# Kernel optimization log

Measured on AMD Instinct MI355X. Metric: run time of the kernel, lower is better.

The kernel has to match this reference:

```python
import jax, jax.numpy as jnp
import numpy as np

EPS = 1e-5

def _ste(x, q):
    # straight-through estimator: forward = q, backward = identity
    return x + jax.lax.stop_gradient(q - x)

def quant_act_int4(x):
    # per-token absmax quantization to int4 range [-8, 7] (dequantized)
    s = jnp.clip(jnp.max(jnp.abs(x), axis=-1, keepdims=True), EPS, None) / 7.0
    q = jnp.clip(jnp.round(x / s), -8.0, 7.0) * s
    return _ste(x, q)

def ternary_weight(w):
    # absmean ternary quantization: scale = mean(|w|), w_q in {-1,0,+1} * scale
    scale = jnp.clip(jnp.mean(jnp.abs(w)), EPS, None)
    t = jnp.clip(jnp.round(w / scale), -1.0, 1.0)
    return _ste(w, t * scale)

def setup_inputs() -> dict:
    key = jax.random.key(0)
    kx, kw = jax.random.split(key)
    in_features, out_features = 4096, 16384
    x = jax.random.normal(kx, (4, 2048, in_features), dtype=jnp.float32)
    # kaiming_uniform_(a=sqrt(5)) -> U(-b, b), b = sqrt(6/((1+5)*fan_in)) = 1/sqrt(fan_in)
    bound = 1.0 / np.sqrt(in_features)
    latent_weight = jax.random.uniform(kw, (out_features, in_features), dtype=jnp.float32,
                                       minval=-bound, maxval=bound)
    return {"x": x, "latent_weight": latent_weight}

def reference(x, latent_weight):
    xq = quant_act_int4(x)                    # (B, S, in)
    w_eff = ternary_weight(latent_weight)     # (out, in)
    return jnp.einsum('bsi,oi->bso', xq, w_eff)
```

## Files before the change

### kernel.cpp

```cpp
#include <hip/hip_runtime.h>
#include <hip/hip_bf16.h>
#include <stdint.h>


#define K_DIM 4096
#define M_DIM 8192
#define N_DIM 16384

typedef int v4i __attribute__((ext_vector_type(4)));

typedef __attribute__((address_space(1))) void gvoid_t;
typedef __attribute__((address_space(3))) void lvoid_t;

__device__ __forceinline__ void gl_lds16(const void* g, void* l) {
    __builtin_amdgcn_global_load_lds((gvoid_t*)(void*)g, (lvoid_t*)l, 16, 0, 0);
}

__global__ __launch_bounds__(256) void wabs_partial_k(const float* __restrict__ w,
                                                      double* __restrict__ part) {
    const long n4 = (long)N_DIM * K_DIM / 4;
    long i = (long)blockIdx.x * blockDim.x + threadIdx.x;
    const long stride = (long)gridDim.x * blockDim.x;
    const float4* w4 = (const float4*)w;
    double s = 0.0;
    for (; i < n4; i += stride) {
        float4 v = w4[i];
        s += (double)fabsf(v.x);
        s += (double)fabsf(v.y);
        s += (double)fabsf(v.z);
        s += (double)fabsf(v.w);
    }
    __shared__ double red[256];
    const int tid = threadIdx.x;
    red[tid] = s;
    __syncthreads();
    for (int w2 = 128; w2 > 0; w2 >>= 1) {
        if (tid < w2) red[tid] += red[tid + w2];
        __syncthreads();
    }
    if (tid == 0) part[blockIdx.x] = red[0];
}

__global__ __launch_bounds__(256) void wscale_final_k(const double* __restrict__ part,
                                                      float* __restrict__ wscale) {
    __shared__ double red[256];
    const int tid = threadIdx.x;
    double s = 0.0;
    for (int i = tid; i < 1024; i += 256) s += part[i];
    red[tid] = s;
    __syncthreads();
    for (int w2 = 128; w2 > 0; w2 >>= 1) {
        if (tid < w2) red[tid] += red[tid + w2];
        __syncthreads();
    }
    if (tid == 0) {
        double mean = red[0] / (double)((long)N_DIM * K_DIM);
        *wscale = fmaxf((float)mean, 1e-5f);
    }
}

__global__ __launch_bounds__(256) void wquant_k(const float* __restrict__ w,
                                                signed char* __restrict__ qw,
                                                const float* __restrict__ wscale) {
    const float sc = *wscale;
    const long i = (long)blockIdx.x * 256 + threadIdx.x;
    const float4* w4 = (const float4*)(w + i * 16);
    union { signed char c[16]; int4 v; } u;
#pragma unroll
    for (int j = 0; j < 4; ++j) {
        float4 v = w4[j];
        u.c[j * 4 + 0] = (signed char)fminf(fmaxf(rintf(v.x / sc), -1.f), 1.f);
        u.c[j * 4 + 1] = (signed char)fminf(fmaxf(rintf(v.y / sc), -1.f), 1.f);
        u.c[j * 4 + 2] = (signed char)fminf(fmaxf(rintf(v.z / sc), -1.f), 1.f);
        u.c[j * 4 + 3] = (signed char)fminf(fmaxf(rintf(v.w / sc), -1.f), 1.f);
    }
    *(int4*)(qw + i * 16) = u.v;
}

__global__ __launch_bounds__(256) void xquant_k(const float* __restrict__ x,
                                                signed char* __restrict__ qx,
                                                float* __restrict__ sx,
                                                const float* __restrict__ wscale) {
    const int row = blockIdx.x;
    const int tid = threadIdx.x;
    const float4* xr = (const float4*)(x + (long)row * K_DIM) + tid * 4;
    float4 v[4];
    float am = 0.f;
#pragma unroll
    for (int j = 0; j < 4; ++j) {
        v[j] = xr[j];
        am = fmaxf(am, fmaxf(fmaxf(fabsf(v[j].x), fabsf(v[j].y)),
                             fmaxf(fabsf(v[j].z), fabsf(v[j].w))));
    }
#pragma unroll
    for (int off = 32; off > 0; off >>= 1) am = fmaxf(am, __shfl_down(am, off));
    __shared__ float wm[4];
    if ((tid & 63) == 0) wm[tid >> 6] = am;
    __syncthreads();
    am = fmaxf(fmaxf(wm[0], wm[1]), fmaxf(wm[2], wm[3]));
    const float s = fmaxf(am, 1e-5f) / 7.0f;
    union { signed char c[16]; int4 q; } u;
#pragma unroll
    for (int j = 0; j < 4; ++j) {
        u.c[j * 4 + 0] = (signed char)fminf(fmaxf(rintf(v[j].x / s), -8.f), 7.f);
        u.c[j * 4 + 1] = (signed char)fminf(fmaxf(rintf(v[j].y / s), -8.f), 7.f);
        u.c[j * 4 + 2] = (signed char)fminf(fmaxf(rintf(v[j].z / s), -8.f), 7.f);
        u.c[j * 4 + 3] = (signed char)fminf(fmaxf(rintf(v[j].w / s), -8.f), 7.f);
    }
    *(int4*)(qx + (long)row * K_DIM + tid * 16) = u.q;
    if (tid == 0) sx[row] = s * (*wscale);
}

__global__ __launch_bounds__(256) void gemm_k(const signed char* __restrict__ qx,
                                              const signed char* __restrict__ qw,
                                              const float* __restrict__ sx,
                                              float* __restrict__ out) {
    __shared__ signed char lA[128 * 64];
    __shared__ signed char lB[128 * 64];

    const int tid  = threadIdx.x;
    const int lane = tid & 63;
    const int wave = tid >> 6;
    const int m0 = blockIdx.x * 128;
    const int n0 = blockIdx.y * 128;
    const int wr = (wave >> 1) * 64;
    const int wc = (wave & 1) * 64;

    const int c0 = tid, c1 = tid + 256;
    const int r0 = c0 >> 2, r1 = c1 >> 2;
    const int g0 = ((c0 & 3) - ((r0 >> 1) & 3)) & 3;
    const int g1 = ((c1 & 3) - ((r1 >> 1) & 3)) & 3;
    const signed char* gA0 = qx + (long)(m0 + r0) * K_DIM + g0 * 16;
    const signed char* gA1 = qx + (long)(m0 + r1) * K_DIM + g1 * 16;
    const signed char* gB0 = qw + (long)(n0 + r0) * K_DIM + g0 * 16;
    const signed char* gB1 = qw + (long)(n0 + r1) * K_DIM + g1 * 16;
    signed char* lA0 = &lA[c0 * 16];
    signed char* lA1 = &lA[c1 * 16];
    signed char* lB0 = &lB[c0 * 16];
    signed char* lB1 = &lB[c1 * 16];

    const int fr = lane & 15;
    const int fq = lane >> 4;
    int offA[4], offB[4];
#pragma unroll
    for (int i = 0; i < 4; ++i) {
        int ra = wr + i * 16 + fr;
        offA[i] = ra * 64 + (((fq + (ra >> 1)) & 3) << 4);
        int rb = wc + i * 16 + fr;
        offB[i] = rb * 64 + (((fq + (rb >> 1)) & 3) << 4);
    }

    v4i acc[4][4];
#pragma unroll
    for (int i = 0; i < 4; ++i)
#pragma unroll
        for (int j = 0; j < 4; ++j) acc[i][j] = 0;

    for (int k0 = 0; k0 < K_DIM; k0 += 64) {
        __syncthreads();
        gl_lds16(gA0 + k0, lA0);
        gl_lds16(gA1 + k0, lA1);
        gl_lds16(gB0 + k0, lB0);
        gl_lds16(gB1 + k0, lB1);
        __syncthreads();

        v4i a[4], b[4];
#pragma unroll
        for (int i = 0; i < 4; ++i) a[i] = *(const v4i*)&lA[offA[i]];
#pragma unroll
        for (int i = 0; i < 4; ++i) b[i] = *(const v4i*)&lB[offB[i]];
#pragma unroll
        for (int i = 0; i < 4; ++i)
#pragma unroll
            for (int j = 0; j < 4; ++j)
                acc[i][j] = __builtin_amdgcn_mfma_i32_16x16x64_i8(a[i], b[j], acc[i][j], 0, 0, 0);
    }

#pragma unroll
    for (int i = 0; i < 4; ++i) {
#pragma unroll
        for (int r = 0; r < 4; ++r) {
            const int m = m0 + wr + i * 16 + fq * 4 + r;
            const float sm = sx[m];
#pragma unroll
            for (int j = 0; j < 4; ++j) {
                const int n = n0 + wc + j * 16 + fr;
                out[(long)m * N_DIM + n] = (float)acc[i][j][r] * sm;
            }
        }
    }
}

extern "C" void kernel_launch(void* const* d_in, const int* in_sizes, int n_in,
                              void* d_out, int out_size, void* d_ws, size_t ws_size,
                              hipStream_t stream) {
    const float* x = (const float*)d_in[0];
    const float* w = (const float*)d_in[1];
    float* out = (float*)d_out;
    char* ws = (char*)d_ws;

    double* part         = (double*)(ws);
    float*  wscale       = (float*)(ws + 8192);
    float*  sx           = (float*)(ws + 16384);
    signed char* qx      = (signed char*)(ws + 65536);
    signed char* qw      = (signed char*)(ws + 65536 + (size_t)33554432);

    wabs_partial_k<<<1024, 256, 0, stream>>>(w, part);
    wscale_final_k<<<1, 256, 0, stream>>>(part, wscale);
    wquant_k<<<16384, 256, 0, stream>>>(w, qw, wscale);
    xquant_k<<<8192, 256, 0, stream>>>(x, qx, sx, wscale);
    dim3 grid(M_DIM / 128, N_DIM / 128);
    gemm_k<<<grid, 256, 0, stream>>>(qx, qw, sx, out);
}
```

Baseline: 1.409 ms.

## Enlarge GEMM tile to 256x256 with 8 waves and grid-stride weight quantization

```diff
diff --git a/kernel.cpp b/kernel.cpp
--- a/kernel.cpp
+++ b/kernel.cpp
@@ -63,18 +63,20 @@
                                                 signed char* __restrict__ qw,
                                                 const float* __restrict__ wscale) {
     const float sc = *wscale;
-    const long i = (long)blockIdx.x * 256 + threadIdx.x;
-    const float4* w4 = (const float4*)(w + i * 16);
-    union { signed char c[16]; int4 v; } u;
-#pragma unroll
-    for (int j = 0; j < 4; ++j) {
-        float4 v = w4[j];
-        u.c[j * 4 + 0] = (signed char)fminf(fmaxf(rintf(v.x / sc), -1.f), 1.f);
-        u.c[j * 4 + 1] = (signed char)fminf(fmaxf(rintf(v.y / sc), -1.f), 1.f);
-        u.c[j * 4 + 2] = (signed char)fminf(fmaxf(rintf(v.z / sc), -1.f), 1.f);
-        u.c[j * 4 + 3] = (signed char)fminf(fmaxf(rintf(v.w / sc), -1.f), 1.f);
-    }
-    *(int4*)(qw + i * 16) = u.v;
+    const long stride = (long)gridDim.x * blockDim.x;
+    long i = (long)blockIdx.x * blockDim.x + threadIdx.x;
+    const long n4 = (long)N_DIM * K_DIM / 4;
+    const float4* w4 = (const float4*)w;
+    int* q4 = (int*)qw;
+    for (; i < n4; i += stride) {
+        float4 v = w4[i];
+        union { signed char c[4]; int q; } u;
+        u.c[0] = (signed char)fminf(fmaxf(rintf(v.x / sc), -1.f), 1.f);
+        u.c[1] = (signed char)fminf(fmaxf(rintf(v.y / sc), -1.f), 1.f);
+        u.c[2] = (signed char)fminf(fmaxf(rintf(v.z / sc), -1.f), 1.f);
+        u.c[3] = (signed char)fminf(fmaxf(rintf(v.w / sc), -1.f), 1.f);
+        q4[i] = u.q;
+    }
 }
 
 __global__ __launch_bounds__(256) void xquant_k(const float* __restrict__ x,
@@ -111,68 +113,74 @@
     if (tid == 0) sx[row] = s * (*wscale);
 }
 
-__global__ __launch_bounds__(256) void gemm_k(const signed char* __restrict__ qx,
-                                              const signed char* __restrict__ qw,
-                                              const float* __restrict__ sx,
-                                              float* __restrict__ out) {
-    __shared__ signed char lA[128 * 64];
-    __shared__ signed char lB[128 * 64];
+__global__ __launch_bounds__(512, 2) void gemm_k(const signed char* __restrict__ qx,
+                                                 const signed char* __restrict__ qw,
+                                                 const float* __restrict__ sx,
+                                                 float* __restrict__ out) {
+    __shared__ signed char lA[256 * 64];
+    __shared__ signed char lB[256 * 64];
 
     const int tid  = threadIdx.x;
     const int lane = tid & 63;
     const int wave = tid >> 6;
-    const int m0 = blockIdx.x * 128;
-    const int n0 = blockIdx.y * 128;
+    const int m0 = blockIdx.x * 256;
+    const int n0 = blockIdx.y * 256;
     const int wr = (wave >> 1) * 64;
-    const int wc = (wave & 1) * 64;
-
-    const int c0 = tid, c1 = tid + 256;
-    const int r0 = c0 >> 2, r1 = c1 >> 2;
-    const int g0 = ((c0 & 3) - ((r0 >> 1) & 3)) & 3;
-    const int g1 = ((c1 & 3) - ((r1 >> 1) & 3)) & 3;
-    const signed char* gA0 = qx + (long)(m0 + r0) * K_DIM + g0 * 16;
-    const signed char* gA1 = qx + (long)(m0 + r1) * K_DIM + g1 * 16;
-    const signed char* gB0 = qw + (long)(n0 + r0) * K_DIM + g0 * 16;
-    const signed char* gB1 = qw + (long)(n0 + r1) * K_DIM + g1 * 16;
-    signed char* lA0 = &lA[c0 * 16];
-    signed char* lA1 = &lA[c1 * 16];
-    signed char* lB0 = &lB[c0 * 16];
-    signed char* lB1 = &lB[c1 * 16];
+    const int wc = (wave & 1) * 128;
+
+    const signed char* gsrc[4];
+    signed char* ldst[4];
+#pragma unroll
+    for (int s = 0; s < 4; ++s) {
+        const int c = tid + 512 * s;
+        const int ci = c & 1023;
+        const int r = ci >> 2;
+        const int p = ci & 3;
+        const int g = (p - ((r >> 1) & 3)) & 3;
+        if (c < 1024) {
+            gsrc[s] = qx + (long)(m0 + r) * K_DIM + g * 16;
+            ldst[s] = &lA[ci * 16];
+        } else {
+            gsrc[s] = qw + (long)(n0 + r) * K_DIM + g * 16;
+            ldst[s] = &lB[ci * 16];
+        }
+    }
 
     const int fr = lane & 15;
     const int fq = lane >> 4;
-    int offA[4], offB[4];
+    int offA[4], offB[8];
 #pragma unroll
     for (int i = 0; i < 4; ++i) {
-        int ra = wr + i * 16 + fr;
+        const int ra = wr + i * 16 + fr;
         offA[i] = ra * 64 + (((fq + (ra >> 1)) & 3) << 4);
-        int rb = wc + i * 16 + fr;
-        offB[i] = rb * 64 + (((fq + (rb >> 1)) & 3) << 4);
-    }
-
-    v4i acc[4][4];
+    }
+#pragma unroll
+    for (int j = 0; j < 8; ++j) {
+        const int rb = wc + j * 16 + fr;
+        offB[j] = rb * 64 + (((fq + (rb >> 1)) & 3) << 4);
+    }
+
+    v4i acc[4][8];
 #pragma unroll
     for (int i = 0; i < 4; ++i)
 #pragma unroll
-        for (int j = 0; j < 4; ++j) acc[i][j] = 0;
+        for (int j = 0; j < 8; ++j) acc[i][j] = 0;
 
     for (int k0 = 0; k0 < K_DIM; k0 += 64) {
         __syncthreads();
-        gl_lds16(gA0 + k0, lA0);
-        gl_lds16(gA1 + k0, lA1);
-        gl_lds16(gB0 + k0, lB0);
-        gl_lds16(gB1 + k0, lB1);
-        __syncthreads();
-
-        v4i a[4], b[4];
+#pragma unroll
+        for (int s = 0; s < 4; ++s) gl_lds16(gsrc[s] + k0, ldst[s]);
+        __syncthreads();
+
+        v4i a[4], b[8];
 #pragma unroll
         for (int i = 0; i < 4; ++i) a[i] = *(const v4i*)&lA[offA[i]];
 #pragma unroll
-        for (int i = 0; i < 4; ++i) b[i] = *(const v4i*)&lB[offB[i]];
+        for (int j = 0; j < 8; ++j) b[j] = *(const v4i*)&lB[offB[j]];
 #pragma unroll
         for (int i = 0; i < 4; ++i)
 #pragma unroll
-            for (int j = 0; j < 4; ++j)
+            for (int j = 0; j < 8; ++j)
                 acc[i][j] = __builtin_amdgcn_mfma_i32_16x16x64_i8(a[i], b[j], acc[i][j], 0, 0, 0);
     }
 
@@ -183,7 +191,7 @@
             const int m = m0 + wr + i * 16 + fq * 4 + r;
             const float sm = sx[m];
 #pragma unroll
-            for (int j = 0; j < 4; ++j) {
+            for (int j = 0; j < 8; ++j) {
                 const int n = n0 + wc + j * 16 + fr;
                 out[(long)m * N_DIM + n] = (float)acc[i][j][r] * sm;
             }
@@ -209,6 +217,6 @@
     wscale_final_k<<<1, 256, 0, stream>>>(part, wscale);
     wquant_k<<<16384, 256, 0, stream>>>(w, qw, wscale);
     xquant_k<<<8192, 256, 0, stream>>>(x, qx, sx, wscale);
-    dim3 grid(M_DIM / 128, N_DIM / 128);
-    gemm_k<<<grid, 256, 0, stream>>>(qx, qw, sx, out);
-}
+    dim3 grid(M_DIM / 256, N_DIM / 256);
+    gemm_k<<<grid, 512, 0, stream>>>(qx, qw, sx, out);
+}
```

Measured after the change: 1.425 ms. Within noise of the previous version (+1.1%).
